# Kernel tuning notes

Hardware: AMD Instinct MI355X
Metric: run time of the kernel (lower is better)

Reference implementation:

```python
import jax, jax.numpy as jnp
import numpy as np

CAPS_N, DIMS_N, ROUNDS = 10, 16, 3
IN_CAPS_N, IN_DIMS_N = 1152, 8
BATCH = 256
EPS = 1e-7  # keras backend.epsilon()


def squash(x, axis=-1):
    sq = jnp.sum(x * x, axis=axis, keepdims=True)
    return (sq / (1.0 + sq)) * x / jnp.sqrt(sq + EPS)


def setup_inputs() -> dict:
    key = jax.random.key(0)
    k1, k2 = jax.random.split(key)
    inputs = jax.random.normal(k1, (BATCH, IN_CAPS_N, IN_DIMS_N), dtype=jnp.float32)
    # glorot-ish scale for the transform weights
    W = jax.random.normal(k2, (CAPS_N, IN_CAPS_N, DIMS_N, IN_DIMS_N), dtype=jnp.float32) * 0.05
    return {"inputs": inputs, "W": W}


def reference(inputs, W):
    # u_hat[b,j,i,d] = W[j,i] @ inputs[b,i]  (per-pair prediction vectors)
    u_hat = jnp.einsum('jide,bie->bjid', W, inputs)  # [B, caps_n, in_caps_n, dims_n]
    B = inputs.shape[0]
    cc = jnp.zeros((B, CAPS_N, IN_CAPS_N), dtype=u_hat.dtype)  # routing logits
    v = None
    for r in range(ROUNDS):
        c = jax.nn.softmax(cc, axis=1)                    # softmax over output capsules
        s = jnp.einsum('bji,bjid->bjd', c, u_hat)         # weighted sum over input caps
        v = squash(s, axis=-1)                            # [B, caps_n, dims_n]
        if r != ROUNDS - 1:
            cc = cc + jnp.einsum('bjid,bjd->bji', u_hat, v)  # agreement
    return v
```

## Files before the change

### kernel.cpp

```cpp
#include <hip/hip_runtime.h>

#define B_N 256
#define IC_N 1152
#define J_N 10
#define D_N 16

typedef __attribute__((ext_vector_type(8))) short short8;
typedef __attribute__((ext_vector_type(4))) float floatx4;

union u4s8 { uint4 u; short8 s; };

__device__ __forceinline__ float bf_lo(unsigned int u){
  union { unsigned int i; float f; } c; c.i = u << 16; return c.f;
}
__device__ __forceinline__ float bf_hi(unsigned int u){
  union { unsigned int i; float f; } c; c.i = u & 0xffff0000u; return c.f;
}
__device__ __forceinline__ unsigned int rne16(float f){
  union { float ff; unsigned int i; } c; c.ff = f;
  return (c.i + 0x7FFFu + ((c.i >> 16) & 1u)) >> 16;
}
__device__ __forceinline__ unsigned int pack_rne(float lo, float hi){
  return rne16(lo) | (rne16(hi) << 16);
}
__device__ __forceinline__ unsigned int pack_trunc(float lo, float hi){
  union { float f; unsigned int u; } a, b; a.f = lo; b.f = hi;
  return __builtin_amdgcn_perm(b.u, a.u, 0x07060302u);
}

__global__ __launch_bounds__(256) void caps_prep(
    const float* __restrict__ W, const float* __restrict__ x,
    uint4* __restrict__ wsf, uint4* __restrict__ wcc2,
    uint4* __restrict__ xbf_ib, uint4* __restrict__ xbf_bi,
    float* __restrict__ vsum)
{
  const int tid = threadIdx.x;
  if (blockIdx.x < 720) {
    __shared__ unsigned int lw[1024];
    const int j = blockIdx.x / 72, itile = blockIdx.x % 72;
    const float4* Wt = (const float4*)(W + ((size_t)(j * IC_N + itile * 16) << 7));
    #pragma unroll
    for (int h = 0; h < 2; ++h) {
      const float4 f = Wt[h * 256 + tid];
      lw[(h * 256 + tid) * 2]     = pack_rne(f.x, f.y);
      lw[(h * 256 + tid) * 2 + 1] = pack_rne(f.z, f.w);
    }
    __syncthreads();
    {
      const int ktl = tid >> 6, ln = tid & 63;
      const int base = (ktl * 4 + (ln >> 4)) * 64 + (ln & 15) * 4;
      uint4 q;
      q.x = lw[base]; q.y = lw[base + 1]; q.z = lw[base + 2]; q.w = lw[base + 3];
      wsf[((size_t)j * 288 + itile * 4 + ktl) * 64 + ln] = q;
    }
    {
      const int e = tid >> 5, lane2 = tid & 31;
      const int il = lane2 & 15, dbase = (lane2 >> 4) * 8;
      unsigned short h[8];
      #pragma unroll
      for (int k = 0; k < 8; ++k) {
        const unsigned int u = lw[il * 64 + (dbase + k) * 4 + (e >> 1)];
        h[k] = (e & 1) ? (unsigned short)(u >> 16) : (unsigned short)(u & 0xffffu);
      }
      uint4 q;
      q.x = h[0] | ((unsigned int)h[1] << 16);
      q.y = h[2] | ((unsigned int)h[3] << 16);
      q.z = h[4] | ((unsigned int)h[5] << 16);
      q.w = h[6] | ((unsigned int)h[7] << 16);
      wcc2[(((size_t)j * 8 + e) * 72 + itile) * 32 + lane2] = q;
    }
  } else {
    __shared__ unsigned int tx[4][64 * 17];
    const int xb = blockIdx.x - 720;
    const int t0 = xb * 256 + tid;
    if (t0 < B_N * J_N * D_N) vsum[t0] = 0.f;
    const int b0 = (xb / 18) * 16;
    const int i0 = (xb % 18) * 64;
    #pragma unroll
    for (int r = 0; r < 4; ++r) {
      const int bl = r * 4 + (tid >> 6);
      const int il = tid & 63;
      const float4* sp = (const float4*)(x + ((size_t)((b0 + bl) * IC_N + i0 + il) << 3));
      const float4 a = sp[0], c = sp[1];
      uint4 q;
      q.x = pack_rne(a.x, a.y); q.y = pack_rne(a.z, a.w);
      q.z = pack_rne(c.x, c.y); q.w = pack_rne(c.z, c.w);
      xbf_bi[(size_t)(b0 + bl) * IC_N + i0 + il] = q;
      tx[0][il * 17 + bl] = q.x; tx[1][il * 17 + bl] = q.y;
      tx[2][il * 17 + bl] = q.z; tx[3][il * 17 + bl] = q.w;
    }
    __syncthreads();
    #pragma unroll
    for (int it = 0; it < 4; ++it) {
      const int p  = it * 256 + tid;
      const int il = p >> 4, bl = p & 15;
      uint4 q;
      q.x = tx[0][il * 17 + bl]; q.y = tx[1][il * 17 + bl];
      q.z = tx[2][il * 17 + bl]; q.w = tx[3][il * 17 + bl];
      xbf_ib[(size_t)(i0 + il) * 256 + b0 + bl] = q;
    }
  }
}

__global__ __launch_bounds__(640, 5) void caps_pass(
    const uint4* __restrict__ xbf_ib, const uint4* __restrict__ xbf_bi,
    const uint4* __restrict__ wsf, const uint4* __restrict__ wcc2,
    const uint4* __restrict__ vsbf, float* __restrict__ s_part, const int round)
{
  __shared__ float ccl[10 * 16 * 17];
  const int tid  = threadIdx.x;
  const int wave = tid >> 6;
  const int lane = tid & 63;
  const int quad = lane >> 4;
  const int col  = lane & 15;
  const int bid  = blockIdx.x;
  const int g    = bid & 7;
  const int rr0  = bid >> 3;
  const int btile = rr0 & 15;
  const int chunk = g * 9 + (rr0 >> 4);
  const int b0 = btile << 4, i0 = chunk << 4;

  uint4 xq[4], wf[4];
  #pragma unroll
  for (int kt = 0; kt < 4; ++kt) {
    const int il = kt * 4 + quad;
    xq[kt] = xbf_ib[(size_t)(i0 + il) * 256 + b0 + col];
    wf[kt] = wsf[((size_t)wave * 288 + (chunk << 2) + kt) * 64 + lane];
  }

  if (round > 0) {
    short8 av = {0,0,0,0,0,0,0,0};
    if (quad < 2)
      av = *(const short8*)&vsbf[((size_t)(b0 + col) * J_N + wave) * 2 + quad];
    uint4 bvq[8];
    #pragma unroll
    for (int e = 0; e < 8; ++e) {
      uint4 q = {0u, 0u, 0u, 0u};
      if (lane < 32)
        q = wcc2[(((size_t)wave * 8 + e) * 72 + chunk) * 32 + lane];
      bvq[e] = q;
    }
    uint4 xr[4];
    #pragma unroll
    for (int r = 0; r < 4; ++r)
      xr[r] = xbf_bi[(size_t)(b0 + quad * 4 + r) * IC_N + i0 + col];
    floatx4 cc4 = {0.f, 0.f, 0.f, 0.f};
    #pragma unroll
    for (int e = 0; e < 8; ++e) {
      u4s8 bv; bv.u = bvq[e];
      floatx4 tf = {0.f, 0.f, 0.f, 0.f};
      tf = __builtin_amdgcn_mfma_f32_16x16x32_bf16(av, bv.s, tf, 0, 0, 0);
      #pragma unroll
      for (int r = 0; r < 4; ++r) {
        const unsigned int u = ((const unsigned int*)&xr[r])[e >> 1];
        const float xe = (e & 1) ? bf_hi(u) : bf_lo(u);
        cc4[r] += tf[r] * xe;
      }
    }
    #pragma unroll
    for (int r = 0; r < 4; ++r)
      ccl[(wave * 16 + col) * 17 + quad * 4 + r] = cc4[r];
    __syncthreads();
    if (tid < 256) {
      const int i = tid >> 4, b = tid & 15;
      float cc[10];
      #pragma unroll
      for (int j = 0; j < 10; ++j) cc[j] = ccl[(j * 16 + i) * 17 + b];
      float m = cc[0];
      #pragma unroll
      for (int j = 1; j < 10; ++j) m = fmaxf(m, cc[j]);
      float den = 0.f;
      #pragma unroll
      for (int j = 0; j < 10; ++j) { cc[j] = __expf(cc[j] - m); den += cc[j]; }
      const float rd = __builtin_amdgcn_rcpf(den);
      #pragma unroll
      for (int j = 0; j < 10; ++j) ccl[(j * 16 + i) * 17 + b] = cc[j] * rd;
    }
    __syncthreads();
  }

  floatx4 acc = {0.f, 0.f, 0.f, 0.f};
  #pragma unroll
  for (int kt = 0; kt < 4; ++kt) {
    const int il = kt * 4 + quad;
    const float c = (round > 0) ? ccl[(wave * 16 + il) * 17 + col] : 0.1f;
    short8 af;
    unsigned int* aq = (unsigned int*)&af;
    aq[0] = pack_trunc(bf_lo(xq[kt].x) * c, bf_hi(xq[kt].x) * c);
    aq[1] = pack_trunc(bf_lo(xq[kt].y) * c, bf_hi(xq[kt].y) * c);
    aq[2] = pack_trunc(bf_lo(xq[kt].z) * c, bf_hi(xq[kt].z) * c);
    aq[3] = pack_trunc(bf_lo(xq[kt].w) * c, bf_hi(xq[kt].w) * c);
    u4s8 bw; bw.u = wf[kt];
    acc = __builtin_amdgcn_mfma_f32_16x16x32_bf16(af, bw.s, acc, 0, 0, 0);
  }
  float* sp = s_part + ((((size_t)btile * 10 + wave) * 16 + quad * 4) * 72
                        + chunk) * 16 + col;
  #pragma unroll
  for (int r = 0; r < 4; ++r) sp[(size_t)r * 72 * 16] = acc[r];
}

__global__ __launch_bounds__(256) void caps_squash(
    const float* __restrict__ s_part, float* __restrict__ vsum,
    unsigned int* __restrict__ vsbf_u, float* __restrict__ out, const int round)
{
  const int tid  = threadIdx.x;
  const int w    = tid >> 6;
  const int lane = tid & 63;
  const int bj   = blockIdx.x * 4 + w;
  const int b    = bj / 10, j = bj - b * 10;
  const int btile = b >> 4, brem = b & 15;
  const float* base = s_part + (((size_t)btile * 10 + j) * 16 + brem) * 1152;
  float acc = 0.f;
  #pragma unroll
  for (int q = 0; q < 18; ++q) acc += base[q * 64 + lane];
  acc += __shfl_xor(acc, 16, 64);
  acc += __shfl_xor(acc, 32, 64);
  const float s = acc;
  float sq = s * s;
  sq += __shfl_xor(sq, 1, 16);
  sq += __shfl_xor(sq, 2, 16);
  sq += __shfl_xor(sq, 4, 16);
  sq += __shfl_xor(sq, 8, 16);
  const float coef = (sq / (1.f + sq)) * rsqrtf(sq + 1e-7f);
  const float v = coef * s;
  if (round < 2) {
    const float vprev = (lane < 16) ? vsum[bj * 16 + lane] : 0.f;
    const float vt = vprev + v;
    const float vtn = __shfl_down(vt, 1, 64);
    if (lane < 16) {
      vsum[bj * 16 + lane] = vt;
      if (!(lane & 1))
        vsbf_u[bj * 8 + (lane >> 1)] = pack_rne(vt, vtn);
    }
  } else if (lane < 16) {
    out[bj * 16 + lane] = v;
  }
}

extern "C" void kernel_launch(void* const* d_in, const int* in_sizes, int n_in,
                              void* d_out, int out_size, void* d_ws, size_t ws_size,
                              hipStream_t stream)
{
  const float* x_p = (const float*)d_in[0];
  const float* W_p = (const float*)d_in[1];

  uint4* wsf    = (uint4*)d_ws;
  uint4* wcc2   = wsf + 184320;
  uint4* xbf_ib = wcc2 + 184320;
  uint4* xbf_bi = xbf_ib + 294912;
  float* s_prt  = (float*)(xbf_bi + 294912);
  float* vsum   = s_prt + 2949120;
  unsigned int* vsbf_u = (unsigned int*)(vsum + 40960);
  float* out_p  = (float*)d_out;

  caps_prep<<<dim3(1008), dim3(256), 0, stream>>>(W_p, x_p, wsf, wcc2,
                                                  xbf_ib, xbf_bi, vsum);
  for (int r = 0; r < 3; ++r) {
    caps_pass<<<dim3(1152), dim3(640), 0, stream>>>(
        xbf_ib, xbf_bi, wsf, wcc2, (const uint4*)vsbf_u, s_prt, r);
    caps_squash<<<dim3(640), dim3(256), 0, stream>>>(
        s_prt, vsum, vsbf_u, out_p, r);
  }
}
```

Baseline: 126.5 us.

## Convert x to bf16 inside routing pass via LDS instead of prep transposes

The prep kernel no longer converts and transposes x into two bf16 layouts. Each caps_pass block now loads its 16x16 fp32 x tile directly, packs it to bf16 in shared memory, and reads both orientations from LDS. This removes the x prep work and its extra global round trip, but each of the three passes reads fp32 x, which is twice the bytes of bf16, and adds a barrier. The grid also becomes 2D (16x72), dropping the swizzled block-to-tile mapping that grouped blocks by chunk.

```diff
diff --git a/kernel.cpp b/kernel.cpp
--- a/kernel.cpp
+++ b/kernel.cpp
@@ -29,104 +29,73 @@
 }
 
 __global__ __launch_bounds__(256) void caps_prep(
-    const float* __restrict__ W, const float* __restrict__ x,
-    uint4* __restrict__ wsf, uint4* __restrict__ wcc2,
-    uint4* __restrict__ xbf_ib, uint4* __restrict__ xbf_bi,
-    float* __restrict__ vsum)
+    const float* __restrict__ W, uint4* __restrict__ wsf,
+    uint4* __restrict__ wcc2, float* __restrict__ vsum)
 {
   const int tid = threadIdx.x;
-  if (blockIdx.x < 720) {
-    __shared__ unsigned int lw[1024];
-    const int j = blockIdx.x / 72, itile = blockIdx.x % 72;
-    const float4* Wt = (const float4*)(W + ((size_t)(j * IC_N + itile * 16) << 7));
-    #pragma unroll
-    for (int h = 0; h < 2; ++h) {
-      const float4 f = Wt[h * 256 + tid];
-      lw[(h * 256 + tid) * 2]     = pack_rne(f.x, f.y);
-      lw[(h * 256 + tid) * 2 + 1] = pack_rne(f.z, f.w);
-    }
-    __syncthreads();
-    {
-      const int ktl = tid >> 6, ln = tid & 63;
-      const int base = (ktl * 4 + (ln >> 4)) * 64 + (ln & 15) * 4;
-      uint4 q;
-      q.x = lw[base]; q.y = lw[base + 1]; q.z = lw[base + 2]; q.w = lw[base + 3];
-      wsf[((size_t)j * 288 + itile * 4 + ktl) * 64 + ln] = q;
-    }
-    {
-      const int e = tid >> 5, lane2 = tid & 31;
-      const int il = lane2 & 15, dbase = (lane2 >> 4) * 8;
-      unsigned short h[8];
-      #pragma unroll
-      for (int k = 0; k < 8; ++k) {
-        const unsigned int u = lw[il * 64 + (dbase + k) * 4 + (e >> 1)];
-        h[k] = (e & 1) ? (unsigned short)(u >> 16) : (unsigned short)(u & 0xffffu);
-      }
-      uint4 q;
-      q.x = h[0] | ((unsigned int)h[1] << 16);
-      q.y = h[2] | ((unsigned int)h[3] << 16);
-      q.z = h[4] | ((unsigned int)h[5] << 16);
-      q.w = h[6] | ((unsigned int)h[7] << 16);
-      wcc2[(((size_t)j * 8 + e) * 72 + itile) * 32 + lane2] = q;
-    }
-  } else {
-    __shared__ unsigned int tx[4][64 * 17];
-    const int xb = blockIdx.x - 720;
-    const int t0 = xb * 256 + tid;
-    if (t0 < B_N * J_N * D_N) vsum[t0] = 0.f;
-    const int b0 = (xb / 18) * 16;
-    const int i0 = (xb % 18) * 64;
-    #pragma unroll
-    for (int r = 0; r < 4; ++r) {
-      const int bl = r * 4 + (tid >> 6);
-      const int il = tid & 63;
-      const float4* sp = (const float4*)(x + ((size_t)((b0 + bl) * IC_N + i0 + il) << 3));
-      const float4 a = sp[0], c = sp[1];
-      uint4 q;
-      q.x = pack_rne(a.x, a.y); q.y = pack_rne(a.z, a.w);
-      q.z = pack_rne(c.x, c.y); q.w = pack_rne(c.z, c.w);
-      xbf_bi[(size_t)(b0 + bl) * IC_N + i0 + il] = q;
-      tx[0][il * 17 + bl] = q.x; tx[1][il * 17 + bl] = q.y;
-      tx[2][il * 17 + bl] = q.z; tx[3][il * 17 + bl] = q.w;
-    }
-    __syncthreads();
-    #pragma unroll
-    for (int it = 0; it < 4; ++it) {
-      const int p  = it * 256 + tid;
-      const int il = p >> 4, bl = p & 15;
-      uint4 q;
-      q.x = tx[0][il * 17 + bl]; q.y = tx[1][il * 17 + bl];
-      q.z = tx[2][il * 17 + bl]; q.w = tx[3][il * 17 + bl];
-      xbf_ib[(size_t)(i0 + il) * 256 + b0 + bl] = q;
-    }
+  const int t0 = blockIdx.x * 256 + tid;
+  if (t0 < B_N * J_N * D_N) vsum[t0] = 0.f;
+  __shared__ unsigned int lw[1024];
+  const int j = blockIdx.x / 72, itile = blockIdx.x % 72;
+  const float4* Wt = (const float4*)(W + ((size_t)(j * IC_N + itile * 16) << 7));
+  #pragma unroll
+  for (int h = 0; h < 2; ++h) {
+    const float4 f = Wt[h * 256 + tid];
+    lw[(h * 256 + tid) * 2]     = pack_rne(f.x, f.y);
+    lw[(h * 256 + tid) * 2 + 1] = pack_rne(f.z, f.w);
+  }
+  __syncthreads();
+  {
+    const int ktl = tid >> 6, ln = tid & 63;
+    const int base = (ktl * 4 + (ln >> 4)) * 64 + (ln & 15) * 4;
+    uint4 q;
+    q.x = lw[base]; q.y = lw[base + 1]; q.z = lw[base + 2]; q.w = lw[base + 3];
+    wsf[((size_t)j * 288 + itile * 4 + ktl) * 64 + ln] = q;
+  }
+  {
+    const int e = tid >> 5, lane2 = tid & 31;
+    const int il = lane2 & 15, dbase = (lane2 >> 4) * 8;
+    unsigned short h[8];
+    #pragma unroll
+    for (int k = 0; k < 8; ++k) {
+      const unsigned int u = lw[il * 64 + (dbase + k) * 4 + (e >> 1)];
+      h[k] = (e & 1) ? (unsigned short)(u >> 16) : (unsigned short)(u & 0xffffu);
+    }
+    uint4 q;
+    q.x = h[0] | ((unsigned int)h[1] << 16);
+    q.y = h[2] | ((unsigned int)h[3] << 16);
+    q.z = h[4] | ((unsigned int)h[5] << 16);
+    q.w = h[6] | ((unsigned int)h[7] << 16);
+    wcc2[(((size_t)j * 8 + e) * 72 + itile) * 32 + lane2] = q;
   }
 }
 
 __global__ __launch_bounds__(640, 5) void caps_pass(
-    const uint4* __restrict__ xbf_ib, const uint4* __restrict__ xbf_bi,
+    const float* __restrict__ x,
     const uint4* __restrict__ wsf, const uint4* __restrict__ wcc2,
     const uint4* __restrict__ vsbf, float* __restrict__ s_part, const int round)
 {
   __shared__ float ccl[10 * 16 * 17];
+  __shared__ unsigned int xt[16 * 17 * 4];
+
   const int tid  = threadIdx.x;
   const int wave = tid >> 6;
   const int lane = tid & 63;
   const int quad = lane >> 4;
   const int col  = lane & 15;
-  const int bid  = blockIdx.x;
-  const int g    = bid & 7;
-  const int rr0  = bid >> 3;
-  const int btile = rr0 & 15;
-  const int chunk = g * 9 + (rr0 >> 4);
-  const int b0 = btile << 4, i0 = chunk << 4;
-
-  uint4 xq[4], wf[4];
-  #pragma unroll
-  for (int kt = 0; kt < 4; ++kt) {
-    const int il = kt * 4 + quad;
-    xq[kt] = xbf_ib[(size_t)(i0 + il) * 256 + b0 + col];
-    wf[kt] = wsf[((size_t)wave * 288 + (chunk << 2) + kt) * 64 + lane];
-  }
+  const int b0   = blockIdx.x << 4;
+  const int i0   = blockIdx.y << 4;
+
+  if (tid < 512) {
+    const int b = tid >> 5, j4 = tid & 31;
+    const int i = j4 >> 1, half = j4 & 1;
+    const float4 v = ((const float4*)(x + ((size_t)((b0 + b) * IC_N + i0 + i) << 3)))[half];
+    const int idx = ((i * 17 + b) << 2) + (half << 1);
+    xt[idx]     = pack_rne(v.x, v.y);
+    xt[idx + 1] = pack_rne(v.z, v.w);
+  }
+  __syncthreads();
+  const uint4* xtq = (const uint4*)xt;
 
   if (round > 0) {
     short8 av = {0,0,0,0,0,0,0,0};
@@ -137,13 +106,13 @@
     for (int e = 0; e < 8; ++e) {
       uint4 q = {0u, 0u, 0u, 0u};
       if (lane < 32)
-        q = wcc2[(((size_t)wave * 8 + e) * 72 + chunk) * 32 + lane];
+        q = wcc2[(((size_t)wave * 8 + e) * 72 + blockIdx.y) * 32 + lane];
       bvq[e] = q;
     }
     uint4 xr[4];
     #pragma unroll
     for (int r = 0; r < 4; ++r)
-      xr[r] = xbf_bi[(size_t)(b0 + quad * 4 + r) * IC_N + i0 + col];
+      xr[r] = xtq[col * 17 + quad * 4 + r];
     floatx4 cc4 = {0.f, 0.f, 0.f, 0.f};
     #pragma unroll
     for (int e = 0; e < 8; ++e) {
@@ -183,18 +152,20 @@
   #pragma unroll
   for (int kt = 0; kt < 4; ++kt) {
     const int il = kt * 4 + quad;
+    const uint4 xq = xtq[il * 17 + col];
+    const uint4 wf = wsf[((size_t)wave * 288 + (blockIdx.y << 2) + kt) * 64 + lane];
     const float c = (round > 0) ? ccl[(wave * 16 + il) * 17 + col] : 0.1f;
     short8 af;
     unsigned int* aq = (unsigned int*)&af;
-    aq[0] = pack_trunc(bf_lo(xq[kt].x) * c, bf_hi(xq[kt].x) * c);
-    aq[1] = pack_trunc(bf_lo(xq[kt].y) * c, bf_hi(xq[kt].y) * c);
-    aq[2] = pack_trunc(bf_lo(xq[kt].z) * c, bf_hi(xq[kt].z) * c);
-    aq[3] = pack_trunc(bf_lo(xq[kt].w) * c, bf_hi(xq[kt].w) * c);
-    u4s8 bw; bw.u = wf[kt];
+    aq[0] = pack_trunc(bf_lo(xq.x) * c, bf_hi(xq.x) * c);
+    aq[1] = pack_trunc(bf_lo(xq.y) * c, bf_hi(xq.y) * c);
+    aq[2] = pack_trunc(bf_lo(xq.z) * c, bf_hi(xq.z) * c);
+    aq[3] = pack_trunc(bf_lo(xq.w) * c, bf_hi(xq.w) * c);
+    u4s8 bw; bw.u = wf;
     acc = __builtin_amdgcn_mfma_f32_16x16x32_bf16(af, bw.s, acc, 0, 0, 0);
   }
-  float* sp = s_part + ((((size_t)btile * 10 + wave) * 16 + quad * 4) * 72
-                        + chunk) * 16 + col;
+  float* sp = s_part + ((((size_t)blockIdx.x * 10 + wave) * 16 + quad * 4) * 72
+                        + blockIdx.y) * 16 + col;
   #pragma unroll
   for (int r = 0; r < 4; ++r) sp[(size_t)r * 72 * 16] = acc[r];
 }
@@ -244,20 +215,17 @@
   const float* x_p = (const float*)d_in[0];
   const float* W_p = (const float*)d_in[1];
 
-  uint4* wsf    = (uint4*)d_ws;
-  uint4* wcc2   = wsf + 184320;
-  uint4* xbf_ib = wcc2 + 184320;
-  uint4* xbf_bi = xbf_ib + 294912;
-  float* s_prt  = (float*)(xbf_bi + 294912);
-  float* vsum   = s_prt + 2949120;
+  uint4* wsf   = (uint4*)d_ws;
+  uint4* wcc2  = wsf + 184320;
+  float* s_prt = (float*)(wcc2 + 184320);
+  float* vsum  = s_prt + 2949120;
   unsigned int* vsbf_u = (unsigned int*)(vsum + 40960);
-  float* out_p  = (float*)d_out;
-
-  caps_prep<<<dim3(1008), dim3(256), 0, stream>>>(W_p, x_p, wsf, wcc2,
-                                                  xbf_ib, xbf_bi, vsum);
+  float* out_p = (float*)d_out;
+
+  caps_prep<<<dim3(720), dim3(256), 0, stream>>>(W_p, wsf, wcc2, vsum);
   for (int r = 0; r < 3; ++r) {
-    caps_pass<<<dim3(1152), dim3(640), 0, stream>>>(
-        xbf_ib, xbf_bi, wsf, wcc2, (const uint4*)vsbf_u, s_prt, r);
+    caps_pass<<<dim3(16, 72), dim3(640), 0, stream>>>(
+        x_p, wsf, wcc2, (const uint4*)vsbf_u, s_prt, r);
     caps_squash<<<dim3(640), dim3(256), 0, stream>>>(
         s_prt, vsum, vsbf_u, out_p, r);
   }
```

Measured after the change: 115.7 us. 1.09x faster.
